# Performance work log

Hardware: AMD Instinct MI355X
Metric: run time of the kernel (lower is better)

## Reference

```python
import jax, jax.numpy as jnp
import numpy as np

B, N, H_DIM = 64, 128, 128
NODE_S, NODE_V = 64, 32            # irreps_node = 64x0e + 32x1o -> dim 160
OUT_S, OUT_V = 32, 16              # out irreps  = 32x0e + 16x1o -> dim 80
RBF, ZEMB, HID, LAT, EDIM, NE = 16, 32, 128, 256, 16, 512
EATT = 4096
CUTOFF = 5.0
MAXZ = 100
NODE_DIM = NODE_S + 3 * NODE_V
OUT_DIM = OUT_S + 3 * OUT_V
WN = NODE_S*OUT_S + NODE_V*OUT_S + NODE_S*OUT_V + NODE_V*OUT_V  # 4608 TP weights per edge
GATE_IN = H_DIM + H_DIM + RBF + 1

def _lin(k, fi, fo):
    return jax.random.normal(k, (fi, fo), jnp.float32) / np.sqrt(fi)

def setup_inputs() -> dict:
    ks = jax.random.split(jax.random.key(0), 24)
    flat = B * N
    att_dist = jax.random.uniform(ks[0], (EATT,), jnp.float32, 0.05, CUTOFF)
    dirs = jax.random.normal(ks[1], (EATT, 3), jnp.float32)
    dirs = dirs / jnp.linalg.norm(dirs, axis=-1, keepdims=True)
    return dict(
        h=jax.random.normal(ks[2], (B, N, H_DIM), jnp.float32),
        h_full=jax.random.normal(ks[3], (B, N, NODE_DIM), jnp.float32),
        z=jax.random.randint(ks[4], (B, N), 1, MAXZ + 1),
        mask=jnp.ones((B, N), bool),
        e_feat=jax.random.normal(ks[5], (NE, EDIM), jnp.float32),
        absorber_index=jax.random.randint(ks[6], (B,), 0, N),
        att_dst=jax.random.randint(ks[7], (EATT,), 0, flat),
        att_dist=att_dist,
        att_vec=dirs * att_dist[:, None],
        w_zemb=jax.random.normal(ks[8], (MAXZ + 1, ZEMB), jnp.float32),
        w1_rad=_lin(ks[9], ZEMB + 1 + RBF, HID), b1_rad=jnp.zeros(HID, jnp.float32),
        w2_rad=_lin(ks[10], HID, WN), b2_rad=jnp.zeros(WN, jnp.float32),
        wg1=_lin(ks[11], GATE_IN, HID), bg1=jnp.zeros(HID, jnp.float32),
        wg2=_lin(ks[12], HID, 1), bg2=jnp.zeros(1, jnp.float32),
        we1=_lin(ks[13], EDIM, HID), be1=jnp.zeros(HID, jnp.float32),
        we2=_lin(ks[14], HID, OUT_S + OUT_V), be2=jnp.ones(OUT_S + OUT_V, jnp.float32),
        wo1=_lin(ks[15], OUT_S + OUT_V, HID), bo1=jnp.zeros(HID, jnp.float32),
        wo2=_lin(ks[16], HID, HID), bo2=jnp.zeros(HID, jnp.float32),
        wo3=_lin(ks[17], HID, LAT), bo3=jnp.zeros(LAT, jnp.float32),
    )

def _core(h, h_full, z, e_feat, absorber_index, att_dst, att_dist, att_vec,
          w_zemb, w1_rad, b1_rad, w2_rad, b2_rad, wg1, bg1, wg2, bg2,
          we1, be1, we2, be2, wo1, bo1, wo2, bo2, wo3, bo3):
    B_, N_, H_ = h.shape
    flat = B_ * N_
    dt = h.dtype
    # scatter edge data into flat (B*N) buffers
    amask = jnp.zeros((flat,), bool).at[att_dst].set(True)
    dflat = jnp.zeros((flat,), dt).at[att_dst].set(att_dist.astype(dt))
    vflat = jnp.zeros((flat, 3), dt).at[att_dst].set(att_vec.astype(dt))
    eps = jnp.maximum(dflat, 1e-8)
    u = vflat / eps[:, None]
    # component-normalized real spherical harmonics, lmax=1: Y0 = 1, Y1 = sqrt(3)*u
    ys = jnp.ones((flat, 1), dt)
    yv = jnp.sqrt(jnp.asarray(3.0, dt)) * u
    # Gaussian RBF on distance
    centers = jnp.linspace(0.0, CUTOFF, RBF).astype(dt)
    width = CUTOFF / (RBF - 1)
    rbf = jnp.exp(-0.5 * ((dflat[:, None] - centers) / width) ** 2)
    zr = w_zemb[z].reshape(flat, ZEMB)
    is_abs = jax.nn.one_hot(absorber_index, N_, dtype=dt)  # (B,N)
    win = jnp.concatenate([zr, is_abs.reshape(flat, 1), rbf], -1)
    tpw = jax.nn.silu(win @ w1_rad + b1_rad) @ w2_rad + b2_rad  # (flat, WN)
    o = 0
    wA = tpw[:, o:o + NODE_S*OUT_S].reshape(flat, NODE_S, OUT_S); o += NODE_S*OUT_S
    wB = tpw[:, o:o + NODE_V*OUT_S].reshape(flat, NODE_V, OUT_S); o += NODE_V*OUT_S
    wC = tpw[:, o:o + NODE_S*OUT_V].reshape(flat, NODE_S, OUT_V); o += NODE_S*OUT_V
    wD = tpw[:, o:o + NODE_V*OUT_V].reshape(flat, NODE_V, OUT_V)
    hf = h_full.reshape(flat, NODE_DIM)
    s1 = hf[:, :NODE_S]
    v1 = hf[:, NODE_S:].reshape(flat, NODE_V, 3)
    norm = 1.0 / np.sqrt(NODE_S + NODE_V)   # TP path (fan-in) normalization
    inv_s3 = 1.0 / np.sqrt(3.0)             # CG(1,1->0) = delta/sqrt(3)
    out_s = (jnp.einsum('ei,eio->eo', s1 * ys, wA)
             + jnp.einsum('eic,ec,eio->eo', v1, yv, wB) * inv_s3) * norm
    out_v = (jnp.einsum('ei,eio->eo', s1, wC)[:, :, None] * yv[:, None, :]
             + jnp.einsum('eic,eio->eoc', v1, wD) * ys[:, :, None]) * norm
    ve = jnp.concatenate([out_s, out_v.reshape(flat, 3 * OUT_V)], -1)
    env = jnp.where(dflat < CUTOFF, 0.5 * (jnp.cos(np.pi * dflat / CUTOFF) + 1.0), 0.0)[:, None]
    ve = ve * env
    # PaiNN-style scalar edge gate
    h_abs = jnp.take_along_axis(h, absorber_index[:, None, None], axis=1)  # (B,1,H)
    gate_in = jnp.concatenate([jnp.broadcast_to(h_abs, (B_, N_, H_)), h,
                               rbf.reshape(B_, N_, RBF), is_abs[..., None]], -1)
    gate = jax.nn.sigmoid(jax.nn.silu(gate_in @ wg1 + bg1) @ wg2 + bg2).reshape(flat, 1)
    ve = ve * gate * amask[:, None].astype(dt)
    v_abs = ve.reshape(B_, N_, OUT_DIM).sum(1)  # (B, OUT_DIM)
    # energy irrep modulation: per-mul scalar from energy features
    scales = jax.nn.silu(e_feat @ we1 + be1) @ we2 + be2  # (nE, OUT_S+OUT_V)
    scale_full = jnp.concatenate([scales[:, :OUT_S], jnp.repeat(scales[:, OUT_S:], 3, axis=-1)], -1)
    v_mod = v_abs[:, None, :] * scale_full[None]  # (B, nE, OUT_DIM)
    vecs = v_mod[..., OUT_S:].reshape(B_, scales.shape[0], OUT_V, 3)
    inv = jnp.concatenate([v_mod[..., :OUT_S], jnp.sqrt(jnp.sum(vecs * vecs, -1) + 1e-12)], -1)
    x = jax.nn.silu(inv @ wo1 + bo1)
    x = jax.nn.silu(x @ wo2 + bo2)
    return x @ wo3 + bo3  # (B, nE, LAT)

def reference(h, h_full, z, mask, e_feat, absorber_index, att_dst, att_dist, att_vec,
              w_zemb, w1_rad, b1_rad, w2_rad, b2_rad, wg1, bg1, wg2, bg2,
              we1, be1, we2, be2, wo1, bo1, wo2, bo2, wo3, bo3):
    # mask is computed into att_mask in the original but never used downstream
    return _core(h, h_full, z, e_feat, absorber_index, att_dst, att_dist, att_vec,
                 w_zemb, w1_rad, b1_rad, w2_rad, b2_rad, wg1, bg1, wg2, bg2,
                 we1, be1, we2, be2, wo1, bo1, wo2, bo2, wo3, bo3)
```

## Files before the change

### kernel.cpp

```cpp
#include <hip/hip_runtime.h>
#include <math.h>

#define FLAT   8192
#define NB     64
#define OD_    80
#define NE_    512
#define EATT_  4096
#define MAXACT 4096
#define ACCW 96

typedef __bf16 v8bf __attribute__((ext_vector_type(8)));
typedef float  v4f  __attribute__((ext_vector_type(4)));

__device__ __forceinline__ float silu_f(float x) { return x / (1.f + __expf(-x)); }
__device__ __forceinline__ float sigm_f(float x) { return 1.f / (1.f + __expf(-x)); }

__device__ __forceinline__ void transpose_split(const float* __restrict__ src, int ld,
                                                int nbase, __bf16* wh, __bf16* wl,
                                                float (*lds)[129]) {
  int t = threadIdx.x;
#pragma unroll
  for (int it = 0; it < 16; ++it) {
    int idx = it * 256 + t;
    int r = idx >> 5, c4 = idx & 31;
    float4 v = *(const float4*)(src + (size_t)r * ld + nbase + c4 * 4);
    lds[r][c4 * 4 + 0] = v.x;
    lds[r][c4 * 4 + 1] = v.y;
    lds[r][c4 * 4 + 2] = v.z;
    lds[r][c4 * 4 + 3] = v.w;
  }
  __syncthreads();
  int n = t >> 1, kh = (t & 1) * 64;
  union { __bf16 b[64]; uint4 u[8]; } H, L;
#pragma unroll
  for (int k = 0; k < 64; ++k) {
    float v = lds[kh + k][n];
    __bf16 hv = (__bf16)v;
    H.b[k] = hv;
    L.b[k] = (__bf16)(v - (float)hv);
  }
  uint4* ph = (uint4*)(wh + (size_t)(nbase + n) * 128 + kh);
  uint4* pl = (uint4*)(wl + (size_t)(nbase + n) * 128 + kh);
#pragma unroll
  for (int i = 0; i < 8; ++i) { ph[i] = H.u[i]; pl[i] = L.u[i]; }
}

__global__ __launch_bounds__(256) void k_prep(
    const float* __restrict__ w2_rad, const float* __restrict__ wo2,
    const float* __restrict__ wo3,
    const int* __restrict__ abs_idx, const float* __restrict__ h,
    const float* __restrict__ wg1,
    const float* __restrict__ e_feat,
    const float* __restrict__ we1, const float* __restrict__ be1,
    const float* __restrict__ we2, const float* __restrict__ be2,
    __bf16* w2rt_h, __bf16* w2rt_l, __bf16* w2t_h, __bf16* w2t_l,
    __bf16* w3t_h, __bf16* w3t_l,
    float* habs_g, float* acc_glob, int* widx, int* count, float* sfull) {
  __shared__ float lds[128][129];
  int bid = blockIdx.x;
  int t = threadIdx.x;
  if (bid < 36) {
    transpose_split(w2_rad, 4608, bid * 128, w2rt_h, w2rt_l, lds);
  } else if (bid < 37) {
    transpose_split(wo2, 128, 0, w2t_h, w2t_l, lds);
  } else if (bid < 39) {
    transpose_split(wo3, 256, (bid - 37) * 128, w3t_h, w3t_l, lds);
  } else if (bid < 71) {
    float* hs = &lds[0][0];
    int half = t >> 7, tt = t & 127;
    int b = (bid - 39) * 2 + half;
    int nabs = abs_idx[b];
    hs[half * 128 + tt] = h[(size_t)(b * 128 + nabs) * 128 + tt];
    __syncthreads();
    float g = 0.f;
    for (int c = 0; c < 128; ++c) g = fmaf(hs[half * 128 + c], wg1[c * 128 + tt], g);
    habs_g[b * 128 + tt] = g;
  } else if (bid < 103) {
    int g = (bid - 71) * 256 + t;
    widx[g] = -1;
    if (g == 0) *count = 0;
    float4* ap = (float4*)(acc_glob + (size_t)g * 48);
    float4 z = make_float4(0.f, 0.f, 0.f, 0.f);
#pragma unroll
    for (int i = 0; i < 12; ++i) ap[i] = z;
  } else {
    float* hid = &lds[0][0];
    int half = t >> 7, tt = t & 127;
    int row = (bid - 103) * 2 + half;
    const float* ef = e_feat + row * 16;
    float s = be1[tt];
    for (int k = 0; k < 16; ++k) s = fmaf(ef[k], we1[k * 128 + tt], s);
    hid[half * 128 + tt] = silu_f(s);
    __syncthreads();
    if (tt < 48) {
      float o = be2[tt];
      for (int k = 0; k < 128; ++k) o = fmaf(hid[half * 128 + k], we2[k * 48 + tt], o);
      if (tt < 32) sfull[row * 80 + tt] = o;
      else {
        int oo = tt - 32;
        sfull[row * 80 + 32 + oo * 3 + 0] = o;
        sfull[row * 80 + 32 + oo * 3 + 1] = o;
        sfull[row * 80 + 32 + oo * 3 + 2] = o;
      }
    }
  }
}

__global__ void k_scatter(const int* __restrict__ att_dst, int* widx) {
  int i = blockIdx.x * 256 + threadIdx.x;
  if (i < EATT_) atomicMax(&widx[att_dst[i]], i);
}

__global__ void k_build(const int* __restrict__ widx, int* active, int* inv, int* count) {
  int j = blockIdx.x * 256 + threadIdx.x;
  if (j < FLAT && widx[j] >= 0) {
    int p = atomicAdd(count, 1);
    active[p] = j;
    inv[j] = p;
  }
}

__global__ __launch_bounds__(128) void k_node4(
    const int* __restrict__ count, const int* __restrict__ active,
    const int* __restrict__ widx,
    const float* __restrict__ att_dist, const float* __restrict__ att_vec,
    const int* __restrict__ z, const float* __restrict__ w_zemb,
    const int* __restrict__ abs_idx,
    const float* __restrict__ w1_rad, const float* __restrict__ b1_rad,
    const float* __restrict__ h, const float* __restrict__ habs_g,
    const float* __restrict__ wg1, const float* __restrict__ bg1,
    const float* __restrict__ wg2, const float* __restrict__ bg2,
    const float* __restrict__ h_full,
    __bf16* ah_glob, __bf16* al_glob,
    float* coef_glob, float* meta_f) {
  int cnt = *count;
  int pbase = blockIdx.x * 4;
  if (pbase >= cnt) return;
  int t = threadIdx.x;

  __shared__ float win[4][49];
  __shared__ float yv_s[4][3];
  __shared__ float sh_d[4];
  __shared__ float red[4][128];
  __shared__ float hsh[4][128];

  bool ok[4];
  int jj[4], ee[4], bb[4];
  float isab[4];
#pragma unroll
  for (int q = 0; q < 4; ++q) {
    int pos = pbase + q;
    ok[q] = pos < cnt;
    jj[q] = ok[q] ? active[pos] : 0;
    ee[q] = ok[q] ? widx[jj[q]] : 0;
    if (ee[q] < 0) ee[q] = 0;
    bb[q] = jj[q] >> 7;
    isab[q] = ((jj[q] & 127) == abs_idx[bb[q]]) ? 1.f : 0.f;
  }

  if (t < 4) {
    int q = t;
    float d = att_dist[ee[q]];
    sh_d[q] = d;
    float eps = fmaxf(d, 1e-8f);
    const float s3 = 1.7320508075688772f;
    yv_s[q][0] = s3 * att_vec[ee[q] * 3 + 0] / eps;
    yv_s[q][1] = s3 * att_vec[ee[q] * 3 + 1] / eps;
    yv_s[q][2] = s3 * att_vec[ee[q] * 3 + 2] / eps;
  }
#pragma unroll
  for (int q = 0; q < 4; ++q) {
    if (t < 32) win[q][t] = w_zemb[z[jj[q]] * 32 + t];
    if (t == 32) win[q][32] = isab[q];
    if (t >= 33 && t < 49) {
      int k = t - 33;
      float d = att_dist[ee[q]];
      float x = (d - (float)k * (1.f / 3.f)) * 3.f;
      win[q][t] = __expf(-0.5f * x * x);
    }
    hsh[q][t] = h[(size_t)jj[q] * 128 + t];
  }
  __syncthreads();

  {
    float s[4];
    float bv = b1_rad[t];
#pragma unroll
    for (int q = 0; q < 4; ++q) s[q] = bv;
    for (int k = 0; k < 49; ++k) {
      float wv = w1_rad[k * 128 + t];
#pragma unroll
      for (int q = 0; q < 4; ++q) s[q] = fmaf(win[q][k], wv, s[q]);
    }
#pragma unroll
    for (int q = 0; q < 4; ++q) {
      if (ok[q]) {
        float av = silu_f(s[q]);
        __bf16 hv = (__bf16)av;
        ah_glob[(size_t)(pbase + q) * 128 + t] = hv;
        al_glob[(size_t)(pbase + q) * 128 + t] = (__bf16)(av - (float)hv);
      }
    }
  }

  {
    float g[4];
#pragma unroll
    for (int q = 0; q < 4; ++q) g[q] = bg1[t] + habs_g[bb[q] * 128 + t];
    for (int c = 0; c < 128; ++c) {
      float wv = wg1[(128 + c) * 128 + t];
#pragma unroll
      for (int q = 0; q < 4; ++q) g[q] = fmaf(hsh[q][c], wv, g[q]);
    }
    for (int k = 0; k < 16; ++k) {
      float wv = wg1[(256 + k) * 128 + t];
#pragma unroll
      for (int q = 0; q < 4; ++q) g[q] = fmaf(win[q][33 + k], wv, g[q]);
    }
    {
      float wv = wg1[272 * 128 + t];
#pragma unroll
      for (int q = 0; q < 4; ++q) g[q] = fmaf(isab[q], wv, g[q]);
    }
    float w2v = wg2[t];
#pragma unroll
    for (int q = 0; q < 4; ++q) red[q][t] = silu_f(g[q]) * w2v;
  }
  __syncthreads();

#pragma unroll
  for (int q = 0; q < 4; ++q) {
    if (!ok[q]) continue;
    int pos = pbase + q;
    const float* hf = h_full + (size_t)jj[q] * 160;
    if (t < 64) coef_glob[pos * 192 + t] = hf[t];
    if (t >= 64 && t < 96) {
      int i = t - 64;
      float pv = hf[64 + i * 3 + 0] * yv_s[q][0] + hf[64 + i * 3 + 1] * yv_s[q][1] +
                 hf[64 + i * 3 + 2] * yv_s[q][2];
      coef_glob[pos * 192 + t] = pv * 0.5773502691896258f;
    }
    if (t < 96) coef_glob[pos * 192 + 96 + t] = hf[64 + t];
  }

  if (t < 4) {
    int q = t;
    if (ok[q]) {
      int pos = pbase + q;
      float tot = 0.f;
      for (int k = 0; k < 128; ++k) tot += red[q][k];
      tot += bg2[0];
      float gate = sigm_f(tot);
      float d = sh_d[q];
      float env = (d < 5.f) ? 0.5f * (__cosf(3.14159265358979323846f * d * 0.2f) + 1.f) : 0.f;
      meta_f[pos * 4 + 0] = yv_s[q][0];
      meta_f[pos * 4 + 1] = yv_s[q][1];
      meta_f[pos * 4 + 2] = yv_s[q][2];
      meta_f[pos * 4 + 3] = gate * env;
    }
  }
}

__global__ __launch_bounds__(256) void k_mrgemm(
    const int* __restrict__ count,
    const __bf16* Ah, const __bf16* Al,
    const __bf16* __restrict__ Bh, const __bf16* __restrict__ Bl,
    const float* __restrict__ b2, const float* __restrict__ coef_glob,
    float* __restrict__ acc_glob) {
  int cc = blockIdx.x;
  int nbase = blockIdx.y * 128;
  int cnt = *count;
  if (nbase >= cnt) return;
  int t = threadIdx.x;
  int w = t >> 6, l = t & 63;
  int kg = l >> 4, ln = l & 15;
  int cbase = cc * 128;

  __shared__ v8bf Bs[2][2][8][64];

  size_t brow0 = (size_t)(cbase + w * 16 + ln) * 128 + kg * 8;
  size_t brow1 = (size_t)(cbase + (w + 4) * 16 + ln) * 128 + kg * 8;
  size_t arow0 = (size_t)(nbase + (2 * w) * 16 + ln) * 128 + kg * 8;
  size_t arow1 = (size_t)(nbase + (2 * w + 1) * 16 + ln) * 128 + kg * 8;

  v8bf rb0 = *(const v8bf*)(Bh + brow0);
  v8bf rb1 = *(const v8bf*)(Bh + brow1);
  v8bf rb2 = *(const v8bf*)(Bl + brow0);
  v8bf rb3 = *(const v8bf*)(Bl + brow1);
  v8bf ah0 = *(const v8bf*)(Ah + arow0);
  v8bf al0 = *(const v8bf*)(Al + arow0);
  v8bf ah1 = *(const v8bf*)(Ah + arow1);
  v8bf al1 = *(const v8bf*)(Al + arow1);
  Bs[0][0][w][l]     = rb0;
  Bs[0][0][w + 4][l] = rb1;
  Bs[0][1][w][l]     = rb2;
  Bs[0][1][w + 4][l] = rb3;
  __syncthreads();

  v4f acc[2][8];
  v4f z4 = {0.f, 0.f, 0.f, 0.f};
#pragma unroll
  for (int i = 0; i < 2; ++i)
#pragma unroll
    for (int j = 0; j < 8; ++j) acc[i][j] = z4;

  for (int kb = 0; kb < 4; ++kb) {
    int cur = kb & 1;
    v8bf nb0, nb1, nb2, nb3, nh0, nl0, nh1, nl1;
    if (kb < 3) {
      int off = (kb + 1) * 32;
      nb0 = *(const v8bf*)(Bh + brow0 + off);
      nb1 = *(const v8bf*)(Bh + brow1 + off);
      nb2 = *(const v8bf*)(Bl + brow0 + off);
      nb3 = *(const v8bf*)(Bl + brow1 + off);
      nh0 = *(const v8bf*)(Ah + arow0 + off);
      nl0 = *(const v8bf*)(Al + arow0 + off);
      nh1 = *(const v8bf*)(Ah + arow1 + off);
      nl1 = *(const v8bf*)(Al + arow1 + off);
    }
#pragma unroll
    for (int nt = 0; nt < 8; ++nt) {
      v8bf bh = Bs[cur][0][nt][l];
      v8bf bl = Bs[cur][1][nt][l];
      acc[0][nt] = __builtin_amdgcn_mfma_f32_16x16x32_bf16(ah0, bh, acc[0][nt], 0, 0, 0);
      acc[0][nt] = __builtin_amdgcn_mfma_f32_16x16x32_bf16(al0, bh, acc[0][nt], 0, 0, 0);
      acc[0][nt] = __builtin_amdgcn_mfma_f32_16x16x32_bf16(ah0, bl, acc[0][nt], 0, 0, 0);
      acc[1][nt] = __builtin_amdgcn_mfma_f32_16x16x32_bf16(ah1, bh, acc[1][nt], 0, 0, 0);
      acc[1][nt] = __builtin_amdgcn_mfma_f32_16x16x32_bf16(al1, bh, acc[1][nt], 0, 0, 0);
      acc[1][nt] = __builtin_amdgcn_mfma_f32_16x16x32_bf16(ah1, bl, acc[1][nt], 0, 0, 0);
    }
    if (kb < 3) {
      int nxt = cur ^ 1;
      Bs[nxt][0][w][l]     = nb0;
      Bs[nxt][0][w + 4][l] = nb1;
      Bs[nxt][1][w][l]     = nb2;
      Bs[nxt][1][w + 4][l] = nb3;
      ah0 = nh0; al0 = nl0; ah1 = nh1; al1 = nl1;
    }
    __syncthreads();
  }

  float b2v[8];
#pragma unroll
  for (int nt = 0; nt < 8; ++nt) b2v[nt] = b2[cbase + nt * 16 + ln];

#pragma unroll
  for (int mi = 0; mi < 2; ++mi) {
    int nodeb = nbase + (2 * w + mi) * 16 + kg * 4;
#pragma unroll
    for (int j = 0; j < 4; ++j) {
      int nd = nodeb + j;
      if (nd >= cnt) continue;
      const float* cf = coef_glob + (size_t)nd * 192;
      float* dst = acc_glob + (size_t)nd * ACCW;
      if (cc < 24) {
        float s0 = 0.f, s1 = 0.f;
#pragma unroll
        for (int m = 0; m < 4; ++m) {
          float c = cf[cc * 4 + m];
          s0 = fmaf(acc[mi][2 * m][j] + b2v[2 * m], c, s0);
          s1 = fmaf(acc[mi][2 * m + 1][j] + b2v[2 * m + 1], c, s1);
        }
        unsafeAtomicAdd(&dst[ln], s0);
        unsafeAtomicAdd(&dst[16 + ln], s1);
      } else if (cc < 32) {
        float s = 0.f;
#pragma unroll
        for (int nt = 0; nt < 8; ++nt)
          s = fmaf(acc[mi][nt][j] + b2v[nt], cf[(cc - 24) * 8 + nt], s);
        unsafeAtomicAdd(&dst[32 + ln], s);
      } else {
        float s0 = 0.f, s1 = 0.f, s2 = 0.f;
#pragma unroll
        for (int nt = 0; nt < 8; ++nt) {
          float x = acc[mi][nt][j] + b2v[nt];
          const float* c3 = cf + 96 + ((cc - 32) * 8 + nt) * 3;
          s0 = fmaf(x, c3[0], s0);
          s1 = fmaf(x, c3[1], s1);
          s2 = fmaf(x, c3[2], s2);
        }
        unsafeAtomicAdd(&dst[48 + ln], s0);
        unsafeAtomicAdd(&dst[48 + 16 + ln], s1);
        unsafeAtomicAdd(&dst[48 + 32 + ln], s2);
      }
    }
  }
}

__global__ __launch_bounds__(256) void k_head(
    const int* __restrict__ widx, const int* __restrict__ inv,
    const float* __restrict__ meta_f, const float* __restrict__ acc_glob,
    const float* __restrict__ sfull,
    const float* __restrict__ wo1, const float* __restrict__ bo1,
    const __bf16* __restrict__ W2h, const __bf16* __restrict__ W2l,
    const float* __restrict__ bo2,
    const __bf16* __restrict__ W3h, const __bf16* __restrict__ W3l,
    const float* __restrict__ bo3,
    float* __restrict__ out) {
  __shared__ __align__(16) char arena[69632];
  float* w_s = (float*)arena;
  float (*invt)[64] = (float(*)[64])(arena + 24576);
  float* va = (float*)(arena + 36864);
  float (*pgrp)[80] = (float(*)[80])(arena + 36864 + 320);
  char* xsh = arena;
  char* xsl = arena + 16384;
  v8bf (*BsB)[2][8][64] = (v8bf(*)[2][8][64])(arena + 36864);
  char* ysh = arena + 36864;
  char* ysl = arena + 53248;
  v8bf (*BsC)[2][8][64] = (v8bf(*)[2][8][64])arena;

  int rbase = blockIdx.x * 64;
  int b = rbase >> 9;
  int e0 = rbase & 511;
  int t = threadIdx.x;

  {
    const float4* wg = (const float4*)wo1;
    float4* ws4 = (float4*)w_s;
#pragma unroll
    for (int it = 0; it < 6; ++it) ws4[t + it * 256] = wg[t + it * 256];

    if (t < 240) {
      int slot = t % 80, grp = t / 80;
      float s = 0.f;
      for (int idx = grp; idx < 128; idx += 3) {
        int j = (b << 7) + idx;
        if (widx[j] < 0) continue;
        int pos = inv[j];
        float sc = meta_f[pos * 4 + 3] * 0.10206207261596577f;
        const float* ac = acc_glob + (size_t)pos * ACCW;
        if (slot < 32) {
          s = fmaf(ac[slot], sc, s);
        } else {
          int o = (slot - 32) / 3, comp = (slot - 32) % 3;
          s = fmaf(ac[32 + o], sc * meta_f[pos * 4 + comp], s);
          s = fmaf(ac[48 + comp * 16 + o], sc, s);
        }
      }
      pgrp[grp][slot] = s;
    }
  }
  __syncthreads();
  if (t < 80) va[t] = pgrp[0][t] + pgrp[1][t] + pgrp[2][t];
  __syncthreads();

  {
    int tx = t & 15, ty = t >> 4;
    int n0 = ty * 4;

    for (int idx = t; idx < 48 * 64; idx += 256) {
      int cd = idx >> 6, r = idx & 63;
      const float* sf = sfull + (size_t)(e0 + r) * 80;
      float v;
      if (cd < 32) v = va[cd] * sf[cd];
      else {
        int base = 32 + (cd - 32) * 3;
        float m0 = va[base + 0] * sf[base + 0];
        float m1 = va[base + 1] * sf[base + 1];
        float m2 = va[base + 2] * sf[base + 2];
        v = sqrtf(m0 * m0 + m1 * m1 + m2 * m2 + 1e-12f);
      }
      invt[cd][r] = v;
    }
    __syncthreads();

    float acc[4][8];
#pragma unroll
    for (int i = 0; i < 4; ++i)
#pragma unroll
      for (int j = 0; j < 8; ++j) acc[i][j] = 0.f;

    for (int k = 0; k < 48; ++k) {
      float4 av  = *(const float4*)&invt[k][n0];
      float4 w0  = *(const float4*)&w_s[k * 128 + tx * 4];
      float4 w1v = *(const float4*)&w_s[k * 128 + 64 + tx * 4];
#pragma unroll
      for (int i = 0; i < 4; ++i) {
        float a = (i == 0) ? av.x : (i == 1) ? av.y : (i == 2) ? av.z : av.w;
        acc[i][0] = fmaf(a, w0.x,  acc[i][0]);
        acc[i][1] = fmaf(a, w0.y,  acc[i][1]);
        acc[i][2] = fmaf(a, w0.z,  acc[i][2]);
        acc[i][3] = fmaf(a, w0.w,  acc[i][3]);
        acc[i][4] = fmaf(a, w1v.x, acc[i][4]);
        acc[i][5] = fmaf(a, w1v.y, acc[i][5]);
        acc[i][6] = fmaf(a, w1v.z, acc[i][6]);
        acc[i][7] = fmaf(a, w1v.w, acc[i][7]);
      }
    }
    __syncthreads();

    float4 bq0 = *(const float4*)(bo1 + tx * 4);
    float4 bq1 = *(const float4*)(bo1 + 64 + tx * 4);
#pragma unroll
    for (int i = 0; i < 4; ++i) {
      int row = n0 + i;
      int sw = (row & 7) << 4;
      float q0[4] = {silu_f(acc[i][0] + bq0.x), silu_f(acc[i][1] + bq0.y),
                     silu_f(acc[i][2] + bq0.z), silu_f(acc[i][3] + bq0.w)};
      float q1[4] = {silu_f(acc[i][4] + bq1.x), silu_f(acc[i][5] + bq1.y),
                     silu_f(acc[i][6] + bq1.z), silu_f(acc[i][7] + bq1.w)};
      union { __bf16 bb[4]; uint2 u; } H, L;
#pragma unroll
      for (int e = 0; e < 4; ++e) {
        __bf16 hv = (__bf16)q0[e];
        H.bb[e] = hv;
        L.bb[e] = (__bf16)(q0[e] - (float)hv);
      }
      *(uint2*)(xsh + ((row * 256 + tx * 8) ^ sw)) = H.u;
      *(uint2*)(xsl + ((row * 256 + tx * 8) ^ sw)) = L.u;
#pragma unroll
      for (int e = 0; e < 4; ++e) {
        __bf16 hv = (__bf16)q1[e];
        H.bb[e] = hv;
        L.bb[e] = (__bf16)(q1[e] - (float)hv);
      }
      *(uint2*)(xsh + ((row * 256 + 128 + tx * 8) ^ sw)) = H.u;
      *(uint2*)(xsl + ((row * 256 + 128 + tx * 8) ^ sw)) = L.u;
    }
  }
  __syncthreads();

  int w = t >> 6, l = t & 63;
  int kg = l >> 4, ln = l & 15;
  {
    int arw = w * 16 + ln;
    int sw = (arw & 7) << 4;
    v8bf axh[4], axl[4];
#pragma unroll
    for (int kb = 0; kb < 4; ++kb) {
      int byt = arw * 256 + kb * 64 + kg * 16;
      axh[kb] = *(v8bf*)(xsh + (byt ^ sw));
      axl[kb] = *(v8bf*)(xsl + (byt ^ sw));
    }
    {
      size_t p0 = (size_t)(w * 16 + ln) * 128 + kg * 8;
      size_t p1 = (size_t)((w + 4) * 16 + ln) * 128 + kg * 8;
      BsB[0][0][w][l]     = *(const v8bf*)(W2h + p0);
      BsB[0][0][w + 4][l] = *(const v8bf*)(W2h + p1);
      BsB[0][1][w][l]     = *(const v8bf*)(W2l + p0);
      BsB[0][1][w + 4][l] = *(const v8bf*)(W2l + p1);
    }
    __syncthreads();

    v4f acc[8];
    v4f z4 = {0.f, 0.f, 0.f, 0.f};
#pragma unroll
    for (int i = 0; i < 8; ++i) acc[i] = z4;

#pragma unroll
    for (int kb = 0; kb < 4; ++kb) {
      int cur = kb & 1;
      v8bf r0, r1, r2, r3;
      if (kb < 3) {
        size_t p0 = (size_t)(w * 16 + ln) * 128 + (kb + 1) * 32 + kg * 8;
        size_t p1 = (size_t)((w + 4) * 16 + ln) * 128 + (kb + 1) * 32 + kg * 8;
        r0 = *(const v8bf*)(W2h + p0);
        r1 = *(const v8bf*)(W2h + p1);
        r2 = *(const v8bf*)(W2l + p0);
        r3 = *(const v8bf*)(W2l + p1);
      }
#pragma unroll
      for (int nt = 0; nt < 8; ++nt) {
        v8bf bh = BsB[cur][0][nt][l];
        v8bf bl = BsB[cur][1][nt][l];
        acc[nt] = __builtin_amdgcn_mfma_f32_16x16x32_bf16(axh[kb], bh, acc[nt], 0, 0, 0);
        acc[nt] = __builtin_amdgcn_mfma_f32_16x16x32_bf16(axl[kb], bh, acc[nt], 0, 0, 0);
        acc[nt] = __builtin_amdgcn_mfma_f32_16x16x32_bf16(axh[kb], bl, acc[nt], 0, 0, 0);
      }
      if (kb < 3) {
        int nxt = cur ^ 1;
        BsB[nxt][0][w][l]     = r0;
        BsB[nxt][0][w + 4][l] = r1;
        BsB[nxt][1][w][l]     = r2;
        BsB[nxt][1][w + 4][l] = r3;
      }
      __syncthreads();
    }

    int r0l = w * 16 + kg * 4;
#pragma unroll
    for (int nt = 0; nt < 8; ++nt) {
      float bv = bo2[nt * 16 + ln];
#pragma unroll
      for (int j = 0; j < 4; ++j) {
        float x = silu_f(acc[nt][j] + bv);
        int row = r0l + j;
        int byt = (row * 256 + (nt * 16 + ln) * 2) ^ ((row & 7) << 4);
        __bf16 hv = (__bf16)x;
        *(__bf16*)(ysh + byt) = hv;
        *(__bf16*)(ysl + byt) = (__bf16)(x - (float)hv);
      }
    }
  }
  __syncthreads();

  {
    int arw = w * 16 + ln;
    int sw = (arw & 7) << 4;
    v8bf ayh[4], ayl[4];
#pragma unroll
    for (int kb = 0; kb < 4; ++kb) {
      int byt = arw * 256 + kb * 64 + kg * 16;
      ayh[kb] = *(v8bf*)(ysh + (byt ^ sw));
      ayl[kb] = *(v8bf*)(ysl + (byt ^ sw));
    }
    __syncthreads();

    for (int ch = 0; ch < 2; ++ch) {
      int cbase = ch * 128;
      {
        size_t p0 = (size_t)(cbase + w * 16 + ln) * 128 + kg * 8;
        size_t p1 = (size_t)(cbase + (w + 4) * 16 + ln) * 128 + kg * 8;
        BsC[0][0][w][l]     = *(const v8bf*)(W3h + p0);
        BsC[0][0][w + 4][l] = *(const v8bf*)(W3h + p1);
        BsC[0][1][w][l]     = *(const v8bf*)(W3l + p0);
        BsC[0][1][w + 4][l] = *(const v8bf*)(W3l + p1);
      }
      __syncthreads();

      v4f acc[8];
      v4f z4 = {0.f, 0.f, 0.f, 0.f};
#pragma unroll
      for (int i = 0; i < 8; ++i) acc[i] = z4;

#pragma unroll
      for (int kb = 0; kb < 4; ++kb) {
        int cur = kb & 1;
        v8bf r0, r1, r2, r3;
        if (kb < 3) {
          size_t p0 = (size_t)(cbase + w * 16 + ln) * 128 + (kb + 1) * 32 + kg * 8;
          size_t p1 = (size_t)(cbase + (w + 4) * 16 + ln) * 128 + (kb + 1) * 32 + kg * 8;
          r0 = *(const v8bf*)(W3h + p0);
          r1 = *(const v8bf*)(W3h + p1);
          r2 = *(const v8bf*)(W3l + p0);
          r3 = *(const v8bf*)(W3l + p1);
        }
#pragma unroll
        for (int nt = 0; nt < 8; ++nt) {
          v8bf bh = BsC[cur][0][nt][l];
          v8bf bl = BsC[cur][1][nt][l];
          acc[nt] = __builtin_amdgcn_mfma_f32_16x16x32_bf16(ayh[kb], bh, acc[nt], 0, 0, 0);
          acc[nt] = __builtin_amdgcn_mfma_f32_16x16x32_bf16(ayl[kb], bh, acc[nt], 0, 0, 0);
          acc[nt] = __builtin_amdgcn_mfma_f32_16x16x32_bf16(ayh[kb], bl, acc[nt], 0, 0, 0);
        }
        if (kb < 3) {
          int nxt = cur ^ 1;
          BsC[nxt][0][w][l]     = r0;
          BsC[nxt][0][w + 4][l] = r1;
          BsC[nxt][1][w][l]     = r2;
          BsC[nxt][1][w + 4][l] = r3;
        }
        __syncthreads();
      }

      int r0g = rbase + w * 16 + kg * 4;
#pragma unroll
      for (int nt = 0; nt < 8; ++nt) {
        float bv = bo3[cbase + nt * 16 + ln];
#pragma unroll
        for (int j = 0; j < 4; ++j) {
          out[(size_t)(r0g + j) * 256 + cbase + nt * 16 + ln] = acc[nt][j] + bv;
        }
      }
    }
  }
}

extern "C" void kernel_launch(void* const* d_in, const int* in_sizes, int n_in,
                              void* d_out, int out_size, void* d_ws, size_t ws_size,
                              hipStream_t stream) {
  const float* h        = (const float*)d_in[0];
  const float* h_full   = (const float*)d_in[1];
  const int*   z        = (const int*)d_in[2];
  const float* e_feat   = (const float*)d_in[4];
  const int*   abs_idx  = (const int*)d_in[5];
  const int*   att_dst  = (const int*)d_in[6];
  const float* att_dist = (const float*)d_in[7];
  const float* att_vec  = (const float*)d_in[8];
  const float* w_zemb   = (const float*)d_in[9];
  const float* w1_rad   = (const float*)d_in[10];
  const float* b1_rad   = (const float*)d_in[11];
  const float* w2_rad   = (const float*)d_in[12];
  const float* b2_rad   = (const float*)d_in[13];
  const float* wg1      = (const float*)d_in[14];
  const float* bg1      = (const float*)d_in[15];
  const float* wg2      = (const float*)d_in[16];
  const float* bg2      = (const float*)d_in[17];
  const float* we1      = (const float*)d_in[18];
  const float* be1      = (const float*)d_in[19];
  const float* we2      = (const float*)d_in[20];
  const float* be2      = (const float*)d_in[21];
  const float* wo1      = (const float*)d_in[22];
  const float* bo1      = (const float*)d_in[23];
  const float* wo2      = (const float*)d_in[24];
  const float* bo2      = (const float*)d_in[25];
  const float* wo3      = (const float*)d_in[26];
  const float* bo3      = (const float*)d_in[27];
  float* out = (float*)d_out;

  float* meta_f  = (float*)d_ws;
  float* sfull   = meta_f + MAXACT * 4;
  float* habs_g  = sfull + NE_ * OD_;
  __bf16* w2t_h  = (__bf16*)(habs_g + NB * 128);
  __bf16* w2t_l  = w2t_h + 128 * 128;
  __bf16* w3t_h  = w2t_l + 128 * 128;
  __bf16* w3t_l  = w3t_h + 256 * 128;
  int* widx   = (int*)(w3t_l + 256 * 128);
  int* active = widx + FLAT;
  int* inv    = active + MAXACT;
  int* count  = inv + FLAT;
  float* big  = (float*)(((size_t)(count + 1) + 255) & ~(size_t)255);
  __bf16* ah_glob  = (__bf16*)big;
  __bf16* al_glob  = ah_glob + MAXACT * 128;
  float* coef_glob = (float*)(al_glob + MAXACT * 128);
  __bf16* w2rt_h   = (__bf16*)(coef_glob + MAXACT * 192);
  __bf16* w2rt_l   = w2rt_h + 4608 * 128;
  float* acc_glob  = (float*)(w2rt_l + 4608 * 128);

  k_prep<<<359, 256, 0, stream>>>(w2_rad, wo2, wo3, abs_idx, h, wg1,
                                  e_feat, we1, be1, we2, be2,
                                  w2rt_h, w2rt_l, w2t_h, w2t_l, w3t_h, w3t_l,
                                  habs_g, acc_glob, widx, count, sfull);
  k_scatter<<<16, 256, 0, stream>>>(att_dst, widx);
  k_build<<<32, 256, 0, stream>>>(widx, active, inv, count);
  k_node4<<<1024, 128, 0, stream>>>(count, active, widx, att_dist, att_vec, z, w_zemb,
                                    abs_idx, w1_rad, b1_rad, h, habs_g, wg1, bg1, wg2, bg2,
                                    h_full, ah_glob, al_glob, coef_glob, meta_f);
  k_mrgemm<<<dim3(36, 32), 256, 0, stream>>>(count, ah_glob, al_glob, w2rt_h, w2rt_l,
                                             b2_rad, coef_glob, acc_glob);
  k_head<<<512, 256, 0, stream>>>(widx, inv, meta_f, acc_glob, sfull, wo1, bo1,
                                  w2t_h, w2t_l, bo2, w3t_h, w3t_l, bo3, out);
}
```

Before: 242.9 us.

## Precompute per-batch absorber vector once in a combine kernel instead of per head block

```diff
diff --git a/kernel.cpp b/kernel.cpp
--- a/kernel.cpp
+++ b/kernel.cpp
@@ -55,7 +55,8 @@
     const float* __restrict__ we2, const float* __restrict__ be2,
     __bf16* w2rt_h, __bf16* w2rt_l, __bf16* w2t_h, __bf16* w2t_l,
     __bf16* w3t_h, __bf16* w3t_l,
-    float* habs_g, float* acc_glob, int* widx, int* count, float* sfull) {
+    float* habs_g, float* acc_glob, float* vabs, int* widx, int* count,
+    float* sfull) {
   __shared__ float lds[128][129];
   int bid = blockIdx.x;
   int t = threadIdx.x;
@@ -79,6 +80,7 @@
     int g = (bid - 71) * 256 + t;
     widx[g] = -1;
     if (g == 0) *count = 0;
+    if (g < NB * OD_) vabs[g] = 0.f;
     float4* ap = (float4*)(acc_glob + (size_t)g * 48);
     float4 z = make_float4(0.f, 0.f, 0.f, 0.f);
 #pragma unroll
@@ -111,12 +113,11 @@
   if (i < EATT_) atomicMax(&widx[att_dst[i]], i);
 }
 
-__global__ void k_build(const int* __restrict__ widx, int* active, int* inv, int* count) {
+__global__ void k_build(const int* __restrict__ widx, int* active, int* count) {
   int j = blockIdx.x * 256 + threadIdx.x;
   if (j < FLAT && widx[j] >= 0) {
     int p = atomicAdd(count, 1);
     active[p] = j;
-    inv[j] = p;
   }
 }
 
@@ -387,10 +388,34 @@
   }
 }
 
+__global__ void k_combine(const int* __restrict__ count, const int* __restrict__ active,
+                          const float* __restrict__ acc_glob,
+                          const float* __restrict__ meta_f, float* vabs) {
+  int t = threadIdx.x;
+  int pos = blockIdx.x * 2 + (t >> 7);
+  int slot = t & 127;
+  if (pos >= *count || slot >= 96) return;
+  float s = acc_glob[(size_t)pos * ACCW + slot];
+  float sc = meta_f[pos * 4 + 3] * 0.10206207261596577f;
+  int b = active[pos] >> 7;
+  float* vb = vabs + b * 80;
+  if (slot < 32) {
+    unsafeAtomicAdd(&vb[slot], s * sc);
+  } else if (slot < 48) {
+    int o = slot - 32;
+    float q = s * sc;
+    unsafeAtomicAdd(&vb[32 + o * 3 + 0], q * meta_f[pos * 4 + 0]);
+    unsafeAtomicAdd(&vb[32 + o * 3 + 1], q * meta_f[pos * 4 + 1]);
+    unsafeAtomicAdd(&vb[32 + o * 3 + 2], q * meta_f[pos * 4 + 2]);
+  } else {
+    int s2 = slot - 48;
+    int comp = s2 >> 4, o = s2 & 15;
+    unsafeAtomicAdd(&vb[32 + o * 3 + comp], s * sc);
+  }
+}
+
 __global__ __launch_bounds__(256) void k_head(
-    const int* __restrict__ widx, const int* __restrict__ inv,
-    const float* __restrict__ meta_f, const float* __restrict__ acc_glob,
-    const float* __restrict__ sfull,
+    const float* __restrict__ vabs, const float* __restrict__ sfull,
     const float* __restrict__ wo1, const float* __restrict__ bo1,
     const __bf16* __restrict__ W2h, const __bf16* __restrict__ W2l,
     const float* __restrict__ bo2,
@@ -401,7 +426,6 @@
   float* w_s = (float*)arena;
   float (*invt)[64] = (float(*)[64])(arena + 24576);
   float* va = (float*)(arena + 36864);
-  float (*pgrp)[80] = (float(*)[80])(arena + 36864 + 320);
   char* xsh = arena;
   char* xsl = arena + 16384;
   v8bf (*BsB)[2][8][64] = (v8bf(*)[2][8][64])(arena + 36864);
@@ -415,38 +439,16 @@
   int t = threadIdx.x;
 
   {
-    const float4* wg = (const float4*)wo1;
-    float4* ws4 = (float4*)w_s;
-#pragma unroll
-    for (int it = 0; it < 6; ++it) ws4[t + it * 256] = wg[t + it * 256];
-
-    if (t < 240) {
-      int slot = t % 80, grp = t / 80;
-      float s = 0.f;
-      for (int idx = grp; idx < 128; idx += 3) {
-        int j = (b << 7) + idx;
-        if (widx[j] < 0) continue;
-        int pos = inv[j];
-        float sc = meta_f[pos * 4 + 3] * 0.10206207261596577f;
-        const float* ac = acc_glob + (size_t)pos * ACCW;
-        if (slot < 32) {
-          s = fmaf(ac[slot], sc, s);
-        } else {
-          int o = (slot - 32) / 3, comp = (slot - 32) % 3;
-          s = fmaf(ac[32 + o], sc * meta_f[pos * 4 + comp], s);
-          s = fmaf(ac[48 + comp * 16 + o], sc, s);
-        }
-      }
-      pgrp[grp][slot] = s;
-    }
-  }
-  __syncthreads();
-  if (t < 80) va[t] = pgrp[0][t] + pgrp[1][t] + pgrp[2][t];
-  __syncthreads();
-
-  {
     int tx = t & 15, ty = t >> 4;
     int n0 = ty * 4;
+    if (t < 80) va[t] = vabs[b * 80 + t];
+    {
+      const float4* wg = (const float4*)wo1;
+      float4* ws4 = (float4*)w_s;
+#pragma unroll
+      for (int it = 0; it < 6; ++it) ws4[t + it * 256] = wg[t + it * 256];
+    }
+    __syncthreads();
 
     for (int idx = t; idx < 48 * 64; idx += 256) {
       int cd = idx >> 6, r = idx & 63;
@@ -699,7 +701,8 @@
   float* out = (float*)d_out;
 
   float* meta_f  = (float*)d_ws;
-  float* sfull   = meta_f + MAXACT * 4;
+  float* vabs    = meta_f + MAXACT * 4;
+  float* sfull   = vabs + NB * OD_;
   float* habs_g  = sfull + NE_ * OD_;
   __bf16* w2t_h  = (__bf16*)(habs_g + NB * 128);
   __bf16* w2t_l  = w2t_h + 128 * 128;
@@ -707,8 +710,7 @@
   __bf16* w3t_l  = w3t_h + 256 * 128;
   int* widx   = (int*)(w3t_l + 256 * 128);
   int* active = widx + FLAT;
-  int* inv    = active + MAXACT;
-  int* count  = inv + FLAT;
+  int* count  = active + MAXACT;
   float* big  = (float*)(((size_t)(count + 1) + 255) & ~(size_t)255);
   __bf16* ah_glob  = (__bf16*)big;
   __bf16* al_glob  = ah_glob + MAXACT * 128;
@@ -720,14 +722,15 @@
   k_prep<<<359, 256, 0, stream>>>(w2_rad, wo2, wo3, abs_idx, h, wg1,
                                   e_feat, we1, be1, we2, be2,
                                   w2rt_h, w2rt_l, w2t_h, w2t_l, w3t_h, w3t_l,
-                                  habs_g, acc_glob, widx, count, sfull);
+                                  habs_g, acc_glob, vabs, widx, count, sfull);
   k_scatter<<<16, 256, 0, stream>>>(att_dst, widx);
-  k_build<<<32, 256, 0, stream>>>(widx, active, inv, count);
+  k_build<<<32, 256, 0, stream>>>(widx, active, count);
   k_node4<<<1024, 128, 0, stream>>>(count, active, widx, att_dist, att_vec, z, w_zemb,
                                     abs_idx, w1_rad, b1_rad, h, habs_g, wg1, bg1, wg2, bg2,
                                     h_full, ah_glob, al_glob, coef_glob, meta_f);
   k_mrgemm<<<dim3(36, 32), 256, 0, stream>>>(count, ah_glob, al_glob, w2rt_h, w2rt_l,
                                              b2_rad, coef_glob, acc_glob);
-  k_head<<<512, 256, 0, stream>>>(widx, inv, meta_f, acc_glob, sfull, wo1, bo1,
-                                  w2t_h, w2t_l, bo2, w3t_h, w3t_l, bo3, out);
-}
+  k_combine<<<2048, 256, 0, stream>>>(count, active, acc_glob, meta_f, vabs);
+  k_head<<<512, 256, 0, stream>>>(vabs, sfull, wo1, bo1, w2t_h, w2t_l, bo2,
+                                  w3t_h, w3t_l, bo3, out);
+}
```

Result: faster. 219.0 us (-9.8%).
